# Optimization experiments

Hardware: AMD Instinct MI355X
Metric: run time of the kernel (lower is better)

The kernel has to match this reference:

```python
import jax, jax.numpy as jnp
import numpy as np

BETA = 0.9


def setup_inputs() -> dict:
    key = jax.random.key(0)
    ks = jax.random.split(key, 9)
    B, T, D, H, C = 512, 2048, 64, 48, 3
    s = lambda k, shape, fan_in: jax.random.normal(k, shape, jnp.float32) / np.sqrt(fan_in)
    return {
        "x": jax.random.normal(ks[0], (B, T, D), jnp.float32),
        "W_enc": s(ks[1], (H, D), D),
        "b_enc": jnp.zeros((H,), jnp.float32),
        "W_mem": s(ks[2], (H, H), H),
        "b_mem": jnp.zeros((H,), jnp.float32),
        "W_dec": s(ks[3], (D, H), H),
        "b_dec": jnp.zeros((D,), jnp.float32),
        "W_cls": s(ks[4], (C, H), H),
        "b_cls": jnp.zeros((C,), jnp.float32),
    }


def _forward(x, W_enc, b_enc, W_mem, b_mem, W_dec, b_dec, W_cls, b_cls):
    B, T, D = x.shape
    H = W_enc.shape[0]
    # Precompute input drive for all steps in one big matmul: [B, T, H]
    u = jnp.einsum("btd,hd->bth", x, W_enc) + b_enc
    u_t = jnp.swapaxes(u, 0, 1)  # [T, B, H]

    def step(mem, u_step):
        cur = u_step + mem @ W_mem.T + b_mem
        mem = BETA * mem + (1.0 - BETA) * cur
        return mem, jax.nn.sigmoid(mem)

    mem0 = jnp.zeros((B, H), x.dtype)
    _, spikes = jax.lax.scan(step, mem0, u_t)  # spikes: [T, B, H]
    z = jnp.swapaxes(spikes, 0, 1)  # [B, T, H]
    recon = jnp.einsum("bth,dh->btd", z, W_dec) + b_dec
    logits = z.mean(axis=1) @ W_cls.T + b_cls
    return recon, logits, z


def reference(x, W_enc, b_enc, W_mem, b_mem, W_dec, b_dec, W_cls, b_cls):
    return _forward(x, W_enc, b_enc, W_mem, b_mem, W_dec, b_dec, W_cls, b_cls)
```

## Files before the change

### kernel.cpp

```cpp
#include <hip/hip_runtime.h>
#include <cstdint>
#include <cstddef>

#define B_ 512
#define T_ 2048
#define D_ 64
#define H_ 48
#define C_ 3
#define LCH 16
#define KCH 128
#define NC  65536
#define CPB 128

#define RECON_FLOATS ((size_t)B_ * T_ * D_)
#define LOGIT_FLOATS ((size_t)B_ * C_)
#define Z_OFF        (RECON_FLOATS + LOGIT_FLOATS)
#define S0_OFF   ((size_t)50331648)
#define MIN_OFF  ((size_t)53477376)
#define A16_OFF  ((size_t)59768832)

__global__ __launch_bounds__(128) void k_enc(
    const float* __restrict__ x, const float* __restrict__ Wenc,
    const float* __restrict__ benc, const float* __restrict__ bmem,
    float* __restrict__ out)
{
    __shared__ float sx[128][68];
    __shared__ float sw[48][68];
    __shared__ float sbe[48];

    const int tid = threadIdx.x;

    {
        const float4* wf4 = reinterpret_cast<const float4*>(Wenc);
        #pragma unroll
        for (int m = 0; m < 6; ++m) {
            const int idx = tid + 128 * m;
            const int c = idx >> 4, d4 = idx & 15;
            *reinterpret_cast<float4*>(&sw[c][d4 * 4]) = wf4[idx];
        }
    }
    if (tid < 48) sbe[tid] = benc[tid] + bmem[tid];

    {
        const float4* xf4 = reinterpret_cast<const float4*>(x) + (size_t)blockIdx.x * 2048;
        #pragma unroll
        for (int m = 0; m < 16; ++m) {
            const int idx = tid + 128 * m;
            const int row = idx >> 4, d4 = idx & 15;
            *reinterpret_cast<float4*>(&sx[row][d4 * 4]) = xf4[idx];
        }
    }
    __syncthreads();

    const int lane = tid & 63;
    const int wv   = tid >> 6;
    const int rg   = lane >> 2;
    const int cg   = lane & 3;
    const int rowb = wv * 64 + rg;
    const int colb = cg * 12;

    float acc[4][12];
    {
        float bia[12];
        #pragma unroll
        for (int m = 0; m < 3; ++m)
            *reinterpret_cast<float4*>(&bia[4 * m]) = *reinterpret_cast<const float4*>(&sbe[colb + 4 * m]);
        #pragma unroll
        for (int k = 0; k < 4; ++k)
            #pragma unroll
            for (int i = 0; i < 12; ++i) acc[k][i] = bia[i];
    }

    #pragma unroll 2
    for (int d4 = 0; d4 < 16; ++d4) {
        float4 xf[4];
        #pragma unroll
        for (int k = 0; k < 4; ++k)
            xf[k] = *reinterpret_cast<const float4*>(&sx[rowb + 16 * k][d4 * 4]);
        #pragma unroll
        for (int i = 0; i < 12; ++i) {
            const float4 wvv = *reinterpret_cast<const float4*>(&sw[colb + i][d4 * 4]);
            #pragma unroll
            for (int k = 0; k < 4; ++k)
                acc[k][i] = fmaf(xf[k].x, wvv.x, fmaf(xf[k].y, wvv.y,
                             fmaf(xf[k].z, wvv.z, fmaf(xf[k].w, wvv.w, acc[k][i]))));
        }
    }

    const size_t row0 = (size_t)blockIdx.x * 128 + rowb;
    #pragma unroll
    for (int k = 0; k < 4; ++k) {
        float* dst = out + (row0 + 16 * k) * 48 + colb;
        #pragma unroll
        for (int m = 0; m < 3; ++m)
            *reinterpret_cast<float4*>(dst + 4 * m) =
                make_float4(acc[k][4 * m], acc[k][4 * m + 1], acc[k][4 * m + 2], acc[k][4 * m + 3]);
    }
}

__global__ __launch_bounds__(576) void k_powA(
    const float* __restrict__ Wmem, float* __restrict__ out)
{
    __shared__ float a0[48 * 49];
    __shared__ float a1[48 * 49];
    const int tid = threadIdx.x;

    for (int idx = tid; idx < 2304; idx += 576) {
        const int i = idx / 48, j = idx - i * 48;
        a0[i * 49 + j] = 0.1f * Wmem[idx] + (i == j ? 0.9f : 0.0f);
    }
    __syncthreads();

    float* src = a0;
    float* dst = a1;
    #pragma unroll 1
    for (int it = 0; it < 4; ++it) {
        float v[4];
        #pragma unroll
        for (int q = 0; q < 4; ++q) {
            const int o = tid + 576 * q;
            const int i = o / 48, j = o - i * 48;
            float acc = 0.f;
            #pragma unroll
            for (int k = 0; k < 48; ++k)
                acc = fmaf(src[i * 49 + k], src[k * 49 + j], acc);
            v[q] = acc;
        }
        #pragma unroll
        for (int q = 0; q < 4; ++q) {
            const int o = tid + 576 * q;
            const int i = o / 48, j = o - i * 48;
            dst[i * 49 + j] = v[q];
        }
        __syncthreads();
        float* t = src; src = dst; dst = t;
    }
    for (int idx = tid; idx < 2304; idx += 576) {
        const int i = idx / 48, j = idx - i * 48;
        out[A16_OFF + idx] = src[i * 49 + j];
    }
}

#define SCAN_PROLOG                                                             \
    const int tid  = threadIdx.x;                                               \
    for (int idx = tid; idx < 2304; idx += 128) {                               \
        const int i = idx / 48, j = idx - i * 48;                               \
        sA[i * 52 + j] = 0.1f * Wmem[idx] + (i == j ? 0.9f : 0.0f);             \
    }                                                                           \
    const int rowg  = tid >> 4;                                      \
    const int colg  = tid & 15;                                      \
    const int r0    = rowg * 6;                                                 \
    const int cbase = colg * 8;                                                 \
    const size_t c0 = (size_t)blockIdx.x * CPB;

#define LOAD_UREG(sidx)                                                         \
    {                                                                           \
        const float* pb = u + (c0 + cbase) * 768 + (size_t)(sidx) * 48 + r0;    \
        _Pragma("unroll")                                                       \
        for (int j = 0; j < 8; ++j) {                                           \
            _Pragma("unroll")                                                   \
            for (int e = 0; e < 3; ++e) {                                       \
                const float2 v = *reinterpret_cast<const float2*>(pb + j * 768 + 2 * e); \
                ureg[j][2 * e] = v.x; ureg[j][2 * e + 1] = v.y;                 \
            }                                                                   \
        }                                                                       \
    }

#define GEMM_STEP                                                               \
    float acc[6][8];                                                            \
    _Pragma("unroll")                                                           \
    for (int r = 0; r < 6; ++r)                                                 \
        _Pragma("unroll")                                                       \
        for (int j = 0; j < 8; ++j) acc[r][j] = ureg[j][r];                     \
    LOAD_UREG(s + 1 < LCH ? s + 1 : LCH - 1)                                    \
    _Pragma("unroll 2")                                                         \
    for (int k4 = 0; k4 < 12; ++k4) {                                           \
        float4 av[6];                                                           \
        _Pragma("unroll")                                                       \
        for (int r = 0; r < 6; ++r)                                             \
            av[r] = *reinterpret_cast<const float4*>(&sA[(r0 + r) * 52 + k4 * 4]); \
        float4 mv0[4], mv1[4];                                                  \
        _Pragma("unroll")                                                       \
        for (int kk = 0; kk < 4; ++kk) {                                        \
            mv0[kk] = *reinterpret_cast<const float4*>(&sM[(k4 * 4 + kk) * 132 + cbase]);     \
            mv1[kk] = *reinterpret_cast<const float4*>(&sM[(k4 * 4 + kk) * 132 + cbase + 4]); \
        }                                                                       \
        _Pragma("unroll")                                                       \
        for (int kk = 0; kk < 4; ++kk) {                                        \
            _Pragma("unroll")                                                   \
            for (int r = 0; r < 6; ++r) {                                       \
                const float a = kk == 0 ? av[r].x : kk == 1 ? av[r].y           \
                              : kk == 2 ? av[r].z : av[r].w;                    \
                acc[r][0] = fmaf(a, mv0[kk].x, acc[r][0]);                      \
                acc[r][1] = fmaf(a, mv0[kk].y, acc[r][1]);                      \
                acc[r][2] = fmaf(a, mv0[kk].z, acc[r][2]);                      \
                acc[r][3] = fmaf(a, mv0[kk].w, acc[r][3]);                      \
                acc[r][4] = fmaf(a, mv1[kk].x, acc[r][4]);                      \
                acc[r][5] = fmaf(a, mv1[kk].y, acc[r][5]);                      \
                acc[r][6] = fmaf(a, mv1[kk].z, acc[r][6]);                      \
                acc[r][7] = fmaf(a, mv1[kk].w, acc[r][7]);                      \
            }                                                                   \
        }                                                                       \
    }

#define WRITE_M                                                                 \
    __syncthreads();                                                            \
    _Pragma("unroll")                                                           \
    for (int r = 0; r < 6; ++r) {                                               \
        *reinterpret_cast<float4*>(&sM[(r0 + r) * 132 + cbase]) =               \
            make_float4(acc[r][0], acc[r][1], acc[r][2], acc[r][3]);            \
        *reinterpret_cast<float4*>(&sM[(r0 + r) * 132 + cbase + 4]) =           \
            make_float4(acc[r][4], acc[r][5], acc[r][6], acc[r][7]);            \
    }                                                                           \
    __syncthreads();

__global__ __launch_bounds__(128) void k_p1(
    const float* __restrict__ Wmem, const float* __restrict__ u,
    float* __restrict__ s0out)
{
    __shared__ float sA[48 * 52];
    __shared__ float sM[48 * 132];
    SCAN_PROLOG
    for (int idx = tid; idx < 48 * 132; idx += 128) sM[idx] = 0.f;

    float ureg[8][6];
    LOAD_UREG(0)
    __syncthreads();

    #pragma unroll 1
    for (int s = 0; s < LCH; ++s) {
        GEMM_STEP
        WRITE_M
    }

    for (int idx = tid; idx < 48 * CPB; idx += 128) {
        const int c = idx / 48, h = idx - c * 48;
        s0out[(c0 + c) * 48 + h] = sM[h * 132 + c];
    }
}

__global__ __launch_bounds__(64) void k_p2(float* __restrict__ out)
{
    const int lane = threadIdx.x;
    const int b    = blockIdx.x;
    const int h    = lane < H_ ? lane : 0;

    const float* A16 = out + A16_OFF;
    float w16[48];
    #pragma unroll
    for (int j = 0; j < 48; ++j) w16[j] = A16[h * 48 + j];

    float E = 0.f;
    float s0 = out[S0_OFF + (((size_t)b << 7) | 0) * 48 + h];
    #pragma unroll 1
    for (int k = 0; k < KCH; ++k) {
        const size_t c = ((size_t)b << 7) | k;
        if (lane < H_) out[MIN_OFF + c * 48 + h] = E;
        float a0 = s0, a1 = 0.f, a2 = 0.f, a3 = 0.f, a4 = 0.f, a5 = 0.f, a6 = 0.f, a7 = 0.f;
        if (k + 1 < KCH) s0 = out[S0_OFF + (c + 1) * 48 + h];
        #pragma unroll
        for (int g = 0; g < 6; ++g) {
            const int j = 8 * g;
            const float m0 = __int_as_float(__builtin_amdgcn_readlane(__float_as_int(E), j + 0));
            const float m1 = __int_as_float(__builtin_amdgcn_readlane(__float_as_int(E), j + 1));
            const float m2 = __int_as_float(__builtin_amdgcn_readlane(__float_as_int(E), j + 2));
            const float m3 = __int_as_float(__builtin_amdgcn_readlane(__float_as_int(E), j + 3));
            const float m4 = __int_as_float(__builtin_amdgcn_readlane(__float_as_int(E), j + 4));
            const float m5 = __int_as_float(__builtin_amdgcn_readlane(__float_as_int(E), j + 5));
            const float m6 = __int_as_float(__builtin_amdgcn_readlane(__float_as_int(E), j + 6));
            const float m7 = __int_as_float(__builtin_amdgcn_readlane(__float_as_int(E), j + 7));
            a0 = fmaf(m0, w16[j + 0], a0);
            a1 = fmaf(m1, w16[j + 1], a1);
            a2 = fmaf(m2, w16[j + 2], a2);
            a3 = fmaf(m3, w16[j + 3], a3);
            a4 = fmaf(m4, w16[j + 4], a4);
            a5 = fmaf(m5, w16[j + 5], a5);
            a6 = fmaf(m6, w16[j + 6], a6);
            a7 = fmaf(m7, w16[j + 7], a7);
        }
        E = ((a0 + a1) + (a2 + a3)) + ((a4 + a5) + (a6 + a7));
    }
}

__global__ __launch_bounds__(128) void k_p3(
    const float* __restrict__ Wmem, const float* __restrict__ u,
    const float* __restrict__ min_, float* __restrict__ z)
{
    __shared__ float sA[48 * 52];
    __shared__ float sM[48 * 132];
    SCAN_PROLOG
    for (int idx = tid; idx < 48 * CPB; idx += 128) {
        const int c = idx / 48, h = idx - c * 48;
        sM[h * 132 + c] = min_[(c0 + c) * 48 + h];
    }

    float ureg[8][6];
    LOAD_UREG(0)
    __syncthreads();

    const float kExp = -0.14426950408889634f;

    #pragma unroll 1
    for (int s = 0; s < LCH; ++s) {
        GEMM_STEP
        {
            float* zb = z + (c0 + cbase) * 768 + (size_t)s * 48 + r0;
            #pragma unroll
            for (int j = 0; j < 8; ++j) {
                float zq[6];
                #pragma unroll
                for (int r = 0; r < 6; ++r)
                    zq[r] = __builtin_amdgcn_rcpf(1.0f + __builtin_amdgcn_exp2f(acc[r][j] * kExp));
                #pragma unroll
                for (int e = 0; e < 3; ++e)
                    *reinterpret_cast<float2*>(zb + j * 768 + 2 * e) = make_float2(zq[2 * e], zq[2 * e + 1]);
            }
        }
        WRITE_M
    }
}

__global__ __launch_bounds__(64) void k_cls(
    const float* __restrict__ Wcls, const float* __restrict__ bcls,
    float* __restrict__ out)
{
    __shared__ float sz[48];
    const int lane = threadIdx.x;
    const int b    = blockIdx.x;
    const float* zb = out + Z_OFF + (size_t)b * T_ * 48;

    if (lane < 48) {
        float a0 = 0.f, a1 = 0.f, a2 = 0.f, a3 = 0.f;
        #pragma unroll 1
        for (int t = 0; t < T_; t += 32) {
            #pragma unroll
            for (int i = 0; i < 32; i += 4) {
                a0 += zb[(size_t)(t + i + 0) * 48 + lane];
                a1 += zb[(size_t)(t + i + 1) * 48 + lane];
                a2 += zb[(size_t)(t + i + 2) * 48 + lane];
                a3 += zb[(size_t)(t + i + 3) * 48 + lane];
            }
        }
        sz[lane] = (a0 + a1) + (a2 + a3);
    }
    __syncthreads();
    if (lane < C_) {
        float acc = 0.f;
        #pragma unroll
        for (int h = 0; h < 48; ++h) acc = fmaf(sz[h], Wcls[lane * 48 + h], acc);
        out[RECON_FLOATS + (size_t)b * C_ + lane] = acc * (1.0f / (float)T_) + bcls[lane];
    }
}

__global__ __launch_bounds__(256) void k_dec(
    const float* __restrict__ Wdec, const float* __restrict__ bdec,
    float* __restrict__ out)
{
    __shared__ float sz[256][52];
    __shared__ float swT[48][68];
    __shared__ float sbd[64];

    const int tid = threadIdx.x;

    #pragma unroll
    for (int m = 0; m < 12; ++m) {
        const int idx = tid + 256 * m;
        const int d = idx / 48, hh = idx - d * 48;
        swT[hh][d] = Wdec[idx];
    }
    if (tid < 64) sbd[tid] = bdec[tid];

    {
        const float4* zf4 = reinterpret_cast<const float4*>(out + Z_OFF) + (size_t)blockIdx.x * 3072;
        #pragma unroll
        for (int m = 0; m < 12; ++m) {
            const int idx = tid + 256 * m;
            const int row = idx / 12, c4 = idx - row * 12;
            *reinterpret_cast<float4*>(&sz[row][c4 * 4]) = zf4[idx];
        }
    }
    __syncthreads();

    const int lane = tid & 63;
    const int wv   = tid >> 6;
    const int rg   = lane >> 3;
    const int cg   = lane & 7;
    const int rowb = wv * 64 + rg;
    const int colb = cg * 8;

    float acc[8][8];
    {
        float bd[8];
        *reinterpret_cast<float4*>(&bd[0]) = *reinterpret_cast<const float4*>(&sbd[colb]);
        *reinterpret_cast<float4*>(&bd[4]) = *reinterpret_cast<const float4*>(&sbd[colb + 4]);
        #pragma unroll
        for (int k = 0; k < 8; ++k)
            #pragma unroll
            for (int c = 0; c < 8; ++c) acc[k][c] = bd[c];
    }

    #pragma unroll 2
    for (int h4 = 0; h4 < 12; ++h4) {
        float4 zf[8];
        #pragma unroll
        for (int k = 0; k < 8; ++k)
            zf[k] = *reinterpret_cast<const float4*>(&sz[rowb + 8 * k][h4 * 4]);
        #pragma unroll
        for (int j = 0; j < 4; ++j) {
            const float4 w0 = *reinterpret_cast<const float4*>(&swT[h4 * 4 + j][colb]);
            const float4 w1 = *reinterpret_cast<const float4*>(&swT[h4 * 4 + j][colb + 4]);
            #pragma unroll
            for (int k = 0; k < 8; ++k) {
                const float zv = j == 0 ? zf[k].x : (j == 1 ? zf[k].y : (j == 2 ? zf[k].z : zf[k].w));
                acc[k][0] = fmaf(zv, w0.x, acc[k][0]);
                acc[k][1] = fmaf(zv, w0.y, acc[k][1]);
                acc[k][2] = fmaf(zv, w0.z, acc[k][2]);
                acc[k][3] = fmaf(zv, w0.w, acc[k][3]);
                acc[k][4] = fmaf(zv, w1.x, acc[k][4]);
                acc[k][5] = fmaf(zv, w1.y, acc[k][5]);
                acc[k][6] = fmaf(zv, w1.z, acc[k][6]);
                acc[k][7] = fmaf(zv, w1.w, acc[k][7]);
            }
        }
    }

    const size_t row0 = (size_t)blockIdx.x * 256 + rowb;
    #pragma unroll
    for (int k = 0; k < 8; ++k) {
        float* dst = out + (row0 + 8 * k) * 64 + colb;
        *reinterpret_cast<float4*>(dst)     = make_float4(acc[k][0], acc[k][1], acc[k][2], acc[k][3]);
        *reinterpret_cast<float4*>(dst + 4) = make_float4(acc[k][4], acc[k][5], acc[k][6], acc[k][7]);
    }
}

extern "C" void kernel_launch(void* const* d_in, const int* in_sizes, int n_in,
                              void* d_out, int out_size, void* d_ws, size_t ws_size,
                              hipStream_t stream) {
    const float* x    = (const float*)d_in[0];
    const float* Wenc = (const float*)d_in[1];
    const float* benc = (const float*)d_in[2];
    const float* Wmem = (const float*)d_in[3];
    const float* bmem = (const float*)d_in[4];
    const float* Wdec = (const float*)d_in[5];
    const float* bdec = (const float*)d_in[6];
    const float* Wcls = (const float*)d_in[7];
    const float* bcls = (const float*)d_in[8];
    float* out = (float*)d_out;

    k_powA<<<dim3(1), dim3(576), 0, stream>>>(Wmem, out);
    k_enc<<<dim3((B_ * T_) / 128), dim3(128), 0, stream>>>(x, Wenc, benc, bmem, out);
    k_p1<<<dim3(NC / CPB), dim3(128), 0, stream>>>(Wmem, out, out + S0_OFF);
    k_p2<<<dim3(B_), dim3(64), 0, stream>>>(out);
    k_p3<<<dim3(NC / CPB), dim3(128), 0, stream>>>(Wmem, out, out + MIN_OFF, out + Z_OFF);
    k_cls<<<dim3(B_), dim3(64), 0, stream>>>(Wcls, bcls, out);
    k_dec<<<dim3((B_ * T_) / 256), dim3(256), 0, stream>>>(Wdec, bdec, out);
}
```

Baseline: 586.1 us.

## Fuse chunked scan phases and classifier mean into one per-batch kernel

Merges the three scan phases (chunk-local scan, cross-chunk carry propagation via A^16, and the re-scan that emits z) plus the classifier reduction into one kernel, with one block per batch element. Chunk end-states and carry-ins now stay in shared memory instead of round-tripping through global scratch. The classifier sum is accumulated in registers while z is produced, so k_cls no longer re-reads all of z. In exchange, the serial 128-step carry loop now runs on only one wavefront inside each scan block while the other wave waits. The grid is also limited to 512 blocks of 128 threads.

Result: faster. 496.1 us (-15.4%).

```diff
diff --git a/kernel.cpp b/kernel.cpp
--- a/kernel.cpp
+++ b/kernel.cpp
@@ -15,8 +15,6 @@
 #define RECON_FLOATS ((size_t)B_ * T_ * D_)
 #define LOGIT_FLOATS ((size_t)B_ * C_)
 #define Z_OFF        (RECON_FLOATS + LOGIT_FLOATS)
-#define S0_OFF   ((size_t)50331648)
-#define MIN_OFF  ((size_t)53477376)
 #define A16_OFF  ((size_t)59768832)
 
 __global__ __launch_bounds__(128) void k_enc(
@@ -140,18 +138,6 @@
         out[A16_OFF + idx] = src[i * 49 + j];
     }
 }
-
-#define SCAN_PROLOG                                                             \
-    const int tid  = threadIdx.x;                                               \
-    for (int idx = tid; idx < 2304; idx += 128) {                               \
-        const int i = idx / 48, j = idx - i * 48;                               \
-        sA[i * 52 + j] = 0.1f * Wmem[idx] + (i == j ? 0.9f : 0.0f);             \
-    }                                                                           \
-    const int rowg  = tid >> 4;                                      \
-    const int colg  = tid & 15;                                      \
-    const int r0    = rowg * 6;                                                 \
-    const int cbase = colg * 8;                                                 \
-    const size_t c0 = (size_t)blockIdx.x * CPB;
 
 #define LOAD_UREG(sidx)                                                         \
     {                                                                           \
@@ -214,14 +200,31 @@
     }                                                                           \
     __syncthreads();
 
-__global__ __launch_bounds__(128) void k_p1(
-    const float* __restrict__ Wmem, const float* __restrict__ u,
-    float* __restrict__ s0out)
+__global__ __launch_bounds__(128) void k_scan(
+    const float* __restrict__ Wmem, const float* __restrict__ A16g,
+    const float* __restrict__ Wcls, const float* __restrict__ bcls,
+    const float* __restrict__ u, float* __restrict__ z, float* __restrict__ logits)
 {
     __shared__ float sA[48 * 52];
+    __shared__ float sB[48 * 52];
     __shared__ float sM[48 * 132];
-    SCAN_PROLOG
+    __shared__ float szs[48];
+
+    const int tid = threadIdx.x;
+    const int b   = blockIdx.x;
+
+    for (int idx = tid; idx < 2304; idx += 128) {
+        const int i = idx / 48, j = idx - i * 48;
+        sA[i * 52 + j] = 0.1f * Wmem[idx] + (i == j ? 0.9f : 0.0f);
+        sB[i * 52 + j] = A16g[idx];
+    }
     for (int idx = tid; idx < 48 * 132; idx += 128) sM[idx] = 0.f;
+
+    const int rowg  = tid >> 4;
+    const int colg  = tid & 15;
+    const int r0    = rowg * 6;
+    const int cbase = colg * 8;
+    const size_t c0 = (size_t)b * CPB;
 
     float ureg[8][6];
     LOAD_UREG(0)
@@ -233,71 +236,50 @@
         WRITE_M
     }
 
-    for (int idx = tid; idx < 48 * CPB; idx += 128) {
-        const int c = idx / 48, h = idx - c * 48;
-        s0out[(c0 + c) * 48 + h] = sM[h * 132 + c];
-    }
-}
-
-__global__ __launch_bounds__(64) void k_p2(float* __restrict__ out)
-{
-    const int lane = threadIdx.x;
-    const int b    = blockIdx.x;
-    const int h    = lane < H_ ? lane : 0;
-
-    const float* A16 = out + A16_OFF;
-    float w16[48];
+    if (tid < 64) {
+        const int h = tid < 48 ? tid : 0;
+        float w16[48];
+        #pragma unroll
+        for (int j4 = 0; j4 < 12; ++j4) {
+            const float4 w = *reinterpret_cast<const float4*>(&sB[h * 52 + 4 * j4]);
+            w16[4 * j4 + 0] = w.x; w16[4 * j4 + 1] = w.y;
+            w16[4 * j4 + 2] = w.z; w16[4 * j4 + 3] = w.w;
+        }
+        float E = 0.f;
+        #pragma unroll 1
+        for (int k = 0; k < KCH; ++k) {
+            const float s0v = (tid < 48) ? sM[h * 132 + k] : 0.f;
+            if (tid < 48) sM[h * 132 + k] = E;
+            float a0 = s0v, a1 = 0.f, a2 = 0.f, a3 = 0.f, a4 = 0.f, a5 = 0.f, a6 = 0.f, a7 = 0.f;
+            #pragma unroll
+            for (int g = 0; g < 6; ++g) {
+                const int j = 8 * g;
+                const float m0 = __int_as_float(__builtin_amdgcn_readlane(__float_as_int(E), j + 0));
+                const float m1 = __int_as_float(__builtin_amdgcn_readlane(__float_as_int(E), j + 1));
+                const float m2 = __int_as_float(__builtin_amdgcn_readlane(__float_as_int(E), j + 2));
+                const float m3 = __int_as_float(__builtin_amdgcn_readlane(__float_as_int(E), j + 3));
+                const float m4 = __int_as_float(__builtin_amdgcn_readlane(__float_as_int(E), j + 4));
+                const float m5 = __int_as_float(__builtin_amdgcn_readlane(__float_as_int(E), j + 5));
+                const float m6 = __int_as_float(__builtin_amdgcn_readlane(__float_as_int(E), j + 6));
+                const float m7 = __int_as_float(__builtin_amdgcn_readlane(__float_as_int(E), j + 7));
+                a0 = fmaf(m0, w16[j + 0], a0);
+                a1 = fmaf(m1, w16[j + 1], a1);
+                a2 = fmaf(m2, w16[j + 2], a2);
+                a3 = fmaf(m3, w16[j + 3], a3);
+                a4 = fmaf(m4, w16[j + 4], a4);
+                a5 = fmaf(m5, w16[j + 5], a5);
+                a6 = fmaf(m6, w16[j + 6], a6);
+                a7 = fmaf(m7, w16[j + 7], a7);
+            }
+            E = ((a0 + a1) + (a2 + a3)) + ((a4 + a5) + (a6 + a7));
+        }
+    }
+    __syncthreads();
+
+    LOAD_UREG(0)
+    float zrow[6];
     #pragma unroll
-    for (int j = 0; j < 48; ++j) w16[j] = A16[h * 48 + j];
-
-    float E = 0.f;
-    float s0 = out[S0_OFF + (((size_t)b << 7) | 0) * 48 + h];
-    #pragma unroll 1
-    for (int k = 0; k < KCH; ++k) {
-        const size_t c = ((size_t)b << 7) | k;
-        if (lane < H_) out[MIN_OFF + c * 48 + h] = E;
-        float a0 = s0, a1 = 0.f, a2 = 0.f, a3 = 0.f, a4 = 0.f, a5 = 0.f, a6 = 0.f, a7 = 0.f;
-        if (k + 1 < KCH) s0 = out[S0_OFF + (c + 1) * 48 + h];
-        #pragma unroll
-        for (int g = 0; g < 6; ++g) {
-            const int j = 8 * g;
-            const float m0 = __int_as_float(__builtin_amdgcn_readlane(__float_as_int(E), j + 0));
-            const float m1 = __int_as_float(__builtin_amdgcn_readlane(__float_as_int(E), j + 1));
-            const float m2 = __int_as_float(__builtin_amdgcn_readlane(__float_as_int(E), j + 2));
-            const float m3 = __int_as_float(__builtin_amdgcn_readlane(__float_as_int(E), j + 3));
-            const float m4 = __int_as_float(__builtin_amdgcn_readlane(__float_as_int(E), j + 4));
-            const float m5 = __int_as_float(__builtin_amdgcn_readlane(__float_as_int(E), j + 5));
-            const float m6 = __int_as_float(__builtin_amdgcn_readlane(__float_as_int(E), j + 6));
-            const float m7 = __int_as_float(__builtin_amdgcn_readlane(__float_as_int(E), j + 7));
-            a0 = fmaf(m0, w16[j + 0], a0);
-            a1 = fmaf(m1, w16[j + 1], a1);
-            a2 = fmaf(m2, w16[j + 2], a2);
-            a3 = fmaf(m3, w16[j + 3], a3);
-            a4 = fmaf(m4, w16[j + 4], a4);
-            a5 = fmaf(m5, w16[j + 5], a5);
-            a6 = fmaf(m6, w16[j + 6], a6);
-            a7 = fmaf(m7, w16[j + 7], a7);
-        }
-        E = ((a0 + a1) + (a2 + a3)) + ((a4 + a5) + (a6 + a7));
-    }
-}
-
-__global__ __launch_bounds__(128) void k_p3(
-    const float* __restrict__ Wmem, const float* __restrict__ u,
-    const float* __restrict__ min_, float* __restrict__ z)
-{
-    __shared__ float sA[48 * 52];
-    __shared__ float sM[48 * 132];
-    SCAN_PROLOG
-    for (int idx = tid; idx < 48 * CPB; idx += 128) {
-        const int c = idx / 48, h = idx - c * 48;
-        sM[h * 132 + c] = min_[(c0 + c) * 48 + h];
-    }
-
-    float ureg[8][6];
-    LOAD_UREG(0)
-    __syncthreads();
-
+    for (int r = 0; r < 6; ++r) zrow[r] = 0.f;
     const float kExp = -0.14426950408889634f;
 
     #pragma unroll 1
@@ -309,8 +291,10 @@
             for (int j = 0; j < 8; ++j) {
                 float zq[6];
                 #pragma unroll
-                for (int r = 0; r < 6; ++r)
+                for (int r = 0; r < 6; ++r) {
                     zq[r] = __builtin_amdgcn_rcpf(1.0f + __builtin_amdgcn_exp2f(acc[r][j] * kExp));
+                    zrow[r] += zq[r];
+                }
                 #pragma unroll
                 for (int e = 0; e < 3; ++e)
                     *reinterpret_cast<float2*>(zb + j * 768 + 2 * e) = make_float2(zq[2 * e], zq[2 * e + 1]);
@@ -318,37 +302,23 @@
         }
         WRITE_M
     }
-}
-
-__global__ __launch_bounds__(64) void k_cls(
-    const float* __restrict__ Wcls, const float* __restrict__ bcls,
-    float* __restrict__ out)
-{
-    __shared__ float sz[48];
-    const int lane = threadIdx.x;
-    const int b    = blockIdx.x;
-    const float* zb = out + Z_OFF + (size_t)b * T_ * 48;
-
-    if (lane < 48) {
-        float a0 = 0.f, a1 = 0.f, a2 = 0.f, a3 = 0.f;
-        #pragma unroll 1
-        for (int t = 0; t < T_; t += 32) {
-            #pragma unroll
-            for (int i = 0; i < 32; i += 4) {
-                a0 += zb[(size_t)(t + i + 0) * 48 + lane];
-                a1 += zb[(size_t)(t + i + 1) * 48 + lane];
-                a2 += zb[(size_t)(t + i + 2) * 48 + lane];
-                a3 += zb[(size_t)(t + i + 3) * 48 + lane];
-            }
-        }
-        sz[lane] = (a0 + a1) + (a2 + a3);
-    }
-    __syncthreads();
-    if (lane < C_) {
-        float acc = 0.f;
-        #pragma unroll
-        for (int h = 0; h < 48; ++h) acc = fmaf(sz[h], Wcls[lane * 48 + h], acc);
-        out[RECON_FLOATS + (size_t)b * C_ + lane] = acc * (1.0f / (float)T_) + bcls[lane];
+
+    #pragma unroll
+    for (int r = 0; r < 6; ++r)
+        sM[(r0 + r) * 132 + colg] = zrow[r];
+    __syncthreads();
+    if (tid < 48) {
+        float a = 0.f;
+        #pragma unroll
+        for (int c = 0; c < 16; ++c) a += sM[tid * 132 + c];
+        szs[tid] = a;
+    }
+    __syncthreads();
+    if (tid < C_) {
+        float acc2 = 0.f;
+        #pragma unroll
+        for (int hh = 0; hh < 48; ++hh) acc2 = fmaf(szs[hh], Wcls[tid * 48 + hh], acc2);
+        logits[(size_t)b * C_ + tid] = acc2 * (1.0f / (float)T_) + bcls[tid];
     }
 }
 
@@ -449,9 +419,7 @@
 
     k_powA<<<dim3(1), dim3(576), 0, stream>>>(Wmem, out);
     k_enc<<<dim3((B_ * T_) / 128), dim3(128), 0, stream>>>(x, Wenc, benc, bmem, out);
-    k_p1<<<dim3(NC / CPB), dim3(128), 0, stream>>>(Wmem, out, out + S0_OFF);
-    k_p2<<<dim3(B_), dim3(64), 0, stream>>>(out);
-    k_p3<<<dim3(NC / CPB), dim3(128), 0, stream>>>(Wmem, out, out + MIN_OFF, out + Z_OFF);
-    k_cls<<<dim3(B_), dim3(64), 0, stream>>>(Wcls, bcls, out);
+    k_scan<<<dim3(B_), dim3(128), 0, stream>>>(Wmem, out + A16_OFF, Wcls, bcls,
+                                               out, out + Z_OFF, out + RECON_FLOATS);
     k_dec<<<dim3((B_ * T_) / 256), dim3(256), 0, stream>>>(Wdec, bdec, out);
 }
```
